# Performance work log

Hardware: AMD Instinct MI355X
Metric: run time of the kernel (lower is better)

## Reference

```python
import jax, jax.numpy as jnp
import numpy as np

B, S, D = 2, 2048, 1024
H = 16
HD = D // H  # 64


def setup_inputs() -> dict:
    key = jax.random.key(0)
    ks = jax.random.split(key, 5)
    scale = 1.0 / np.sqrt(D)
    return {
        "x": jax.random.normal(ks[0], (B, S, D), dtype=jnp.float32),
        "kqv_w": jax.random.normal(ks[1], (3 * D, D), dtype=jnp.float32) * scale,
        "kqv_b": jnp.zeros((3 * D,), dtype=jnp.float32),
        "out_w": jax.random.normal(ks[2], (D, D), dtype=jnp.float32) * scale,
        "out_b": jnp.zeros((D,), dtype=jnp.float32),
    }


def reference(x, kqv_w, kqv_b, out_w, out_b):
    # x: [B, S, D] -> torch code transposes to [S, B, D] (seq-first)
    xs = jnp.transpose(x, (1, 0, 2))  # [S, B, D]
    qkv = xs @ kqv_w.T + kqv_b        # [S, B, 3D]
    q, k, v = jnp.split(qkv, 3, axis=-1)  # each [S, B, D]

    def to_heads(t):
        # [S, B, D] -> [S, B*H, HD] -> [B*H, S, HD]
        return jnp.transpose(t.reshape(S, B * H, HD), (1, 0, 2))

    q, k, v = to_heads(q), to_heads(k), to_heads(v)
    # NOTE: original module computes self.scaling but never applies it -> no q scaling.
    attn = jnp.einsum('nqd,nkd->nqk', q, k)      # [B*H, S, S]
    attn = jax.nn.softmax(attn, axis=-1)
    out = jnp.einsum('nqk,nkd->nqd', attn, v)    # [B*H, S, HD]
    out = jnp.transpose(out, (1, 0, 2)).reshape(S, B, D)  # [S, B, D]
    out = out @ out_w.T + out_b
    return jnp.transpose(out, (1, 0, 2))  # [B, S, D]
```

## Files before the change

kernel.cpp:

```cpp
#include <hip/hip_runtime.h>

#define SEQ   2048
#define DIM   1024
#define NH    16
#define HD    64
#define BH    32
#define TOK   4096

typedef __bf16 bf16;
typedef __attribute__((ext_vector_type(4))) __bf16 bf16x4;
typedef __attribute__((ext_vector_type(8))) __bf16 bf16x8;
typedef __attribute__((ext_vector_type(4))) float f32x4;

#define LOG2E 1.44269504f

__device__ inline f32x4 mfma16(bf16x8 a, bf16x8 b, f32x4 c) {
  return __builtin_amdgcn_mfma_f32_16x16x32_bf16(a, b, c, 0, 0, 0);
}

__device__ inline void gload_lds16(const bf16* g, bf16* lds) {
  __builtin_amdgcn_global_load_lds(
      (const __attribute__((address_space(1))) void*)g,
      (__attribute__((address_space(3))) void*)lds, 16, 0, 0);
}

__device__ inline float exp2_hw(float x) {
  float r;
  asm("v_exp_f32 %0, %1" : "=v"(r) : "v"(x));
  return r;
}

__device__ inline void split8(const float* src, bf16x8& hi, bf16x8& lo) {
  float4 a = *(const float4*)src;
  float4 b = *(const float4*)(src + 4);
  float f[8] = {a.x, a.y, a.z, a.w, b.x, b.y, b.z, b.w};
#pragma unroll
  for (int i = 0; i < 8; ++i) {
    bf16 h = (bf16)f[i];
    hi[i] = h;
    lo[i] = (bf16)(f[i] - (float)h);
  }
}

__device__ inline void cast8(const float* src, bf16* dst) {
  float4 a = *(const float4*)src;
  float4 b = *(const float4*)(src + 4);
  bf16x8 v;
  v[0] = (bf16)a.x; v[1] = (bf16)a.y; v[2] = (bf16)a.z; v[3] = (bf16)a.w;
  v[4] = (bf16)b.x; v[5] = (bf16)b.y; v[6] = (bf16)b.z; v[7] = (bf16)b.w;
  *(bf16x8*)dst = v;
}

__global__ void prep_kernel(const float* __restrict__ x,
                            const float* __restrict__ kqv_w,
                            const float* __restrict__ out_w,
                            bf16* __restrict__ xh, bf16* __restrict__ xl,
                            bf16* __restrict__ wbf, bf16* __restrict__ wout) {
  const int NX8 = TOK * DIM / 8;
  const int NW8 = 3 * DIM * DIM / 8;
  const int NO8 = DIM * DIM / 8;
  int i = blockIdx.x * 256 + threadIdx.x;
  if (i < NX8) {
    bf16x8 h, l;
    split8(x + (size_t)i * 8, h, l);
    ((bf16x8*)xh)[i] = h;
    ((bf16x8*)xl)[i] = l;
  } else if (i < NX8 + NW8) {
    int j = i - NX8;
    cast8(kqv_w + (size_t)j * 8, wbf + (size_t)j * 8);
  } else if (i < NX8 + NW8 + NO8) {
    int j = i - NX8 - NW8;
    cast8(out_w + (size_t)j * 8, wout + (size_t)j * 8);
  }
}

__global__ __launch_bounds__(256) void gemm_qkv_ps(
    const bf16* __restrict__ xh, const bf16* __restrict__ xl,
    const bf16* __restrict__ wbf, const float* __restrict__ bias,
    bf16* __restrict__ qhh, bf16* __restrict__ qhl, bf16* __restrict__ kh,
    bf16* __restrict__ vT) {
  __shared__ bf16 AhA[64 * 64], AlA[64 * 64], BhA[64 * 64];
  __shared__ bf16 AhB[64 * 64], AlB[64 * 64], BhB[64 * 64];
  const int tid = threadIdx.x;
  const int lane = tid & 63;
  const int wave = tid >> 6;
  const int lr = lane & 15, lk = lane >> 4;
  const int bid = blockIdx.x;
  const int swz = (bid & 7) * 96 + (bid >> 3);
  const int m0 = (swz / 24) * 128, n0 = (swz % 24) * 128;
  const bool two_term = (n0 < DIM);
  const int wm = (wave >> 1) * 64, wn = (wave & 1) * 64;
  f32x4 acc[4][4] = {};

  const int c0i = tid, c1i = 256 + tid;
  const int rp0 = c0i >> 3, lc0 = (c0i & 7) ^ (rp0 & 7);
  const int mm0 = (lc0 >> 2) * 64 + rp0, kk0 = (lc0 & 3) * 8;
  const int rp1 = c1i >> 3, lc1 = (c1i & 7) ^ (rp1 & 7);
  const int mm1 = (lc1 >> 2) * 64 + rp1, kk1 = (lc1 & 3) * 8;
  const bf16* pA0 = xh + (size_t)(m0 + mm0) * DIM + kk0;
  const bf16* pA1 = xh + (size_t)(m0 + mm1) * DIM + kk1;
  const bf16* pL0 = xl + (size_t)(m0 + mm0) * DIM + kk0;
  const bf16* pL1 = xl + (size_t)(m0 + mm1) * DIM + kk1;
  const bf16* pB0 = wbf + (size_t)(n0 + mm0) * DIM + kk0;
  const bf16* pB1 = wbf + (size_t)(n0 + mm1) * DIM + kk1;

  auto stageG = [&](bf16* Ah_, bf16* Al_, bf16* Bh_) {
    gload_lds16(pA0, Ah_ + c0i * 8);
    gload_lds16(pA1, Ah_ + c1i * 8);
    if (two_term) {
      gload_lds16(pL0, Al_ + c0i * 8);
      gload_lds16(pL1, Al_ + c1i * 8);
    }
    gload_lds16(pB0, Bh_ + c0i * 8);
    gload_lds16(pB1, Bh_ + c1i * 8);
    pA0 += 32; pA1 += 32; pL0 += 32; pL1 += 32;
    pB0 += 32; pB1 += 32;
  };

  auto computeG = [&](const bf16* Ah, const bf16* Al, const bf16* Bh) {
    bf16x8 afh[4], afl[4], bfv[4];
#pragma unroll
    for (int i = 0; i < 4; ++i) {
      int m = wm + i * 16 + lr;
      int rp = m & 63;
      int pc = ((m >> 6) * 4 + lk) ^ (rp & 7);
      afh[i] = *(const bf16x8*)(Ah + rp * 64 + pc * 8);
    }
#pragma unroll
    for (int j = 0; j < 4; ++j) {
      int m = wn + j * 16 + lr;
      int rp = m & 63;
      int pc = ((m >> 6) * 4 + lk) ^ (rp & 7);
      bfv[j] = *(const bf16x8*)(Bh + rp * 64 + pc * 8);
    }
    __builtin_amdgcn_s_setprio(1);
#pragma unroll
    for (int i = 0; i < 4; ++i)
#pragma unroll
      for (int j = 0; j < 4; ++j)
        acc[i][j] = mfma16(afh[i], bfv[j], acc[i][j]);
    __builtin_amdgcn_s_setprio(0);
    if (two_term) {
#pragma unroll
      for (int i = 0; i < 4; ++i) {
        int m = wm + i * 16 + lr;
        int rp = m & 63;
        int pc = ((m >> 6) * 4 + lk) ^ (rp & 7);
        afl[i] = *(const bf16x8*)(Al + rp * 64 + pc * 8);
      }
      __builtin_amdgcn_s_setprio(1);
#pragma unroll
      for (int i = 0; i < 4; ++i)
#pragma unroll
        for (int j = 0; j < 4; ++j)
          acc[i][j] = mfma16(afl[i], bfv[j], acc[i][j]);
      __builtin_amdgcn_s_setprio(0);
    }
  };

  stageG(AhA, AlA, BhA);
  __syncthreads();
  for (int k0 = 0; k0 < DIM; k0 += 64) {
    stageG(AhB, AlB, BhB);
    computeG(AhA, AlA, BhA);
    __syncthreads();
    if (k0 + 64 < DIM) {
      stageG(AhA, AlA, BhA);
    }
    computeG(AhB, AlB, BhB);
    __syncthreads();
  }

#pragma unroll
  for (int j = 0; j < 4; ++j) {
    int col = n0 + wn + j * 16 + lr;
    float bv = bias[col];
    int part = col >> 10, cc2 = col & 1023;
    int h = cc2 >> 6, d = cc2 & 63;
#pragma unroll
    for (int i = 0; i < 4; ++i) {
      int rowb = m0 + wm + i * 16 + lk * 4;
#pragma unroll
      for (int r = 0; r < 4; ++r) {
        int row = rowb + r;
        float val = acc[i][j][r] + bv;
        int b = row >> 11, s = row & 2047;
        int n = b * NH + h;
        size_t idx = ((size_t)n * SEQ + s) * HD + d;
        if (part == 0) {
          float vq = val * LOG2E;
          bf16 qh_ = (bf16)vq;
          qhh[idx] = qh_;
          qhl[idx] = (bf16)(vq - (float)qh_);
        } else if (part == 1) {
          kh[idx] = (bf16)val;
        } else {
          vT[((size_t)n * HD + d) * SEQ + s] = (bf16)val;
        }
      }
    }
  }
}

__global__ __launch_bounds__(256) void gemm_out(
    const bf16* __restrict__ A, const bf16* __restrict__ Bw,
    const float* __restrict__ bias, float* __restrict__ outF) {
  __shared__ bf16 AsA[64 * 64], BsA[64 * 64];
  __shared__ bf16 AsB[64 * 64], BsB[64 * 64];
  const int tid = threadIdx.x;
  const int lane = tid & 63;
  const int wave = tid >> 6;
  const int lr = lane & 15, lk = lane >> 4;
  const int bid = blockIdx.x;
  const int swz = (bid & 7) * 32 + (bid >> 3);
  const int m0 = (swz >> 3) * 128, n0 = (swz & 7) * 128;
  const int wm = (wave >> 1) * 64, wn = (wave & 1) * 64;
  f32x4 acc[4][4] = {};

  const int c0i = tid, c1i = 256 + tid;
  const int rp0 = c0i >> 3, lc0 = (c0i & 7) ^ (rp0 & 7);
  const int mm0 = (lc0 >> 2) * 64 + rp0, kk0 = (lc0 & 3) * 8;
  const int rp1 = c1i >> 3, lc1 = (c1i & 7) ^ (rp1 & 7);
  const int mm1 = (lc1 >> 2) * 64 + rp1, kk1 = (lc1 & 3) * 8;
  const bf16* pA0 = A + (size_t)(m0 + mm0) * DIM + kk0;
  const bf16* pA1 = A + (size_t)(m0 + mm1) * DIM + kk1;
  const bf16* pB0 = Bw + (size_t)(n0 + mm0) * DIM + kk0;
  const bf16* pB1 = Bw + (size_t)(n0 + mm1) * DIM + kk1;

#define STAGEO(As_, Bs_)              \
  do {                                \
    gload_lds16(pA0, As_ + c0i * 8);  \
    gload_lds16(pA1, As_ + c1i * 8);  \
    gload_lds16(pB0, Bs_ + c0i * 8);  \
    gload_lds16(pB1, Bs_ + c1i * 8);  \
    pA0 += 32; pA1 += 32;             \
    pB0 += 32; pB1 += 32;             \
  } while (0)

  auto computeO = [&](const bf16* As, const bf16* Bs) {
    bf16x8 af[4], bfv[4];
#pragma unroll
    for (int i = 0; i < 4; ++i) {
      int m = wm + i * 16 + lr;
      int rp = m & 63;
      int pc = ((m >> 6) * 4 + lk) ^ (rp & 7);
      af[i] = *(const bf16x8*)(As + rp * 64 + pc * 8);
    }
#pragma unroll
    for (int j = 0; j < 4; ++j) {
      int m = wn + j * 16 + lr;
      int rp = m & 63;
      int pc = ((m >> 6) * 4 + lk) ^ (rp & 7);
      bfv[j] = *(const bf16x8*)(Bs + rp * 64 + pc * 8);
    }
    __builtin_amdgcn_s_setprio(1);
#pragma unroll
    for (int i = 0; i < 4; ++i)
#pragma unroll
      for (int j = 0; j < 4; ++j)
        acc[i][j] = mfma16(af[i], bfv[j], acc[i][j]);
    __builtin_amdgcn_s_setprio(0);
  };

  STAGEO(AsA, BsA);
  __syncthreads();
  for (int k0 = 0; k0 < DIM; k0 += 64) {
    STAGEO(AsB, BsB);
    computeO(AsA, BsA);
    __syncthreads();
    if (k0 + 64 < DIM) {
      STAGEO(AsA, BsA);
    }
    computeO(AsB, BsB);
    __syncthreads();
  }
#undef STAGEO

#pragma unroll
  for (int j = 0; j < 4; ++j) {
    int col = n0 + wn + j * 16 + lr;
    float bv = bias[col];
#pragma unroll
    for (int i = 0; i < 4; ++i) {
      int rowb = m0 + wm + i * 16 + lk * 4;
#pragma unroll
      for (int r = 0; r < 4; ++r)
        outF[(size_t)(rowb + r) * DIM + col] = acc[i][j][r] + bv;
    }
  }
}

__global__ __launch_bounds__(256) void attn_kernel(
    const bf16* __restrict__ qhh, const bf16* __restrict__ qhl,
    const bf16* __restrict__ kh, const bf16* __restrict__ vT,
    bf16* __restrict__ aout) {
  __shared__ bf16 KsA[64 * 64], VsA[64 * 64];
  __shared__ bf16 KsB[64 * 64], VsB[64 * 64];
  const int tid = threadIdx.x;
  const int lane = tid & 63;
  const int w = tid >> 6;
  const int lr = lane & 15, lk = lane >> 4;
  const int bid = blockIdx.x;
  const int swz = (bid & 7) * 64 + (bid >> 3);
  const int n = swz >> 4;
  const int q0 = (swz & 15) * 128 + w * 32;

  const bf16* qbh = qhh + ((size_t)n * SEQ + q0) * HD;
  const bf16* qbl = qhl + ((size_t)n * SEQ + q0) * HD;
  bf16x8 aqh[2][2], aql[2][2];
#pragma unroll
  for (int g = 0; g < 2; ++g) {
    aqh[g][0] = *(const bf16x8*)(qbh + (g * 16 + lr) * HD + lk * 8);
    aqh[g][1] = *(const bf16x8*)(qbh + (g * 16 + lr) * HD + 32 + lk * 8);
    aql[g][0] = *(const bf16x8*)(qbl + (g * 16 + lr) * HD + lk * 8);
    aql[g][1] = *(const bf16x8*)(qbl + (g * 16 + lr) * HD + 32 + lk * 8);
  }

  const int c0i = tid, c1i = 256 + tid;
  const int r0 = c0i >> 3, lc0 = ((c0i & 7) ^ (r0 & 7)) * 8;
  const int r1 = c1i >> 3, lc1 = ((c1i & 7) ^ (r1 & 7)) * 8;
  const size_t kbase = (size_t)n * SEQ * HD;
  const size_t vbase = (size_t)n * HD * SEQ;
  const bf16* pK0 = kh + kbase + (size_t)r0 * HD + lc0;
  const bf16* pK1 = kh + kbase + (size_t)r1 * HD + lc1;
  const bf16* pV0 = vT + vbase + (size_t)r0 * SEQ + lc0;
  const bf16* pV1 = vT + vbase + (size_t)r1 * SEQ + lc1;
  const bool vsw = (w & 1);

  const int u0v = 2 * (lk >> 1) + (lk & 1);
  const int xr = (2 * (lr & 7)) ^ (lr >> 3);
  const int e0 = ((u0v) ^ xr) * 4;
  const int e1 = ((u0v + 4) ^ xr) * 4;
  const int e2 = ((u0v + 8) ^ xr) * 4;
  const int e3 = ((u0v + 12) ^ xr) * 4;

  bf16x8 ones;
#pragma unroll
  for (int i = 0; i < 8; ++i) ones[i] = (bf16)1.0f;

  f32x4 o[2][4] = {};
  float lrow[2][4] = {};

#define STAGE_K(Ks_)                      \
  do {                                    \
    gload_lds16(pK0, Ks_ + c0i * 8);      \
    gload_lds16(pK1, Ks_ + c1i * 8);      \
    pK0 += 64 * HD; pK1 += 64 * HD;       \
  } while (0)

#define VLOAD(a, b)                       \
  do {                                    \
    a = *(const uint4*)pV0;               \
    b = *(const uint4*)pV1;               \
    pV0 += 64; pV1 += 64;                 \
  } while (0)

#define VWRITE(Vs_, a, b)                                      \
  do {                                                         \
    uint4 t0, t1;                                              \
    if (vsw) {                                                 \
      t0.x = a.z; t0.y = a.w; t0.z = a.x; t0.w = a.y;          \
      t1.x = b.z; t1.y = b.w; t1.z = b.x; t1.w = b.y;          \
    } else { t0 = a; t1 = b; }                                 \
    *(uint4*)((char*)(Vs_) + c0i * 16) = t0;                   \
    *(uint4*)((char*)(Vs_) + c1i * 16) = t1;                   \
  } while (0)

  auto compute = [&](const bf16* Ks, const bf16* Vs) {
    f32x4 sa[2][4] = {};
    __builtin_amdgcn_s_setprio(1);
#pragma unroll
    for (int j = 0; j < 4; ++j) {
      int row = j * 16 + lr;
      int c0 = (lk ^ (row & 7)) * 8;
      int c1 = ((4 + lk) ^ (row & 7)) * 8;
      const bf16* kr = Ks + row * 64;
      bf16x8 b0 = *(const bf16x8*)(kr + c0);
      bf16x8 b1 = *(const bf16x8*)(kr + c1);
#pragma unroll
      for (int g = 0; g < 2; ++g) {
        sa[g][j] = mfma16(b0, aqh[g][0], sa[g][j]);
        sa[g][j] = mfma16(b1, aqh[g][1], sa[g][j]);
        sa[g][j] = mfma16(b0, aql[g][0], sa[g][j]);
        sa[g][j] = mfma16(b1, aql[g][1], sa[g][j]);
      }
    }
    __builtin_amdgcn_s_setprio(0);

    bf16x8 pa[2][2];
#pragma unroll
    for (int g = 0; g < 2; ++g)
#pragma unroll
      for (int jj = 0; jj < 2; ++jj)
#pragma unroll
        for (int r = 0; r < 4; ++r) {
          pa[g][0][jj * 4 + r] = (bf16)exp2_hw(sa[g][jj][r]);
          pa[g][1][jj * 4 + r] = (bf16)exp2_hw(sa[g][2 + jj][r]);
        }

    __builtin_amdgcn_s_setprio(1);
    f32x4 ls[2] = {};
#pragma unroll
    for (int g = 0; g < 2; ++g) {
      ls[g] = mfma16(pa[g][0], ones, ls[g]);
      ls[g] = mfma16(pa[g][1], ones, ls[g]);
    }
#pragma unroll
    for (int dj = 0; dj < 4; ++dj) {
      int row = dj * 16 + lr;
      const bf16* vr = Vs + row * 64;
      bf16x4 v00 = *(const bf16x4*)(vr + e0);
      bf16x4 v01 = *(const bf16x4*)(vr + e1);
      bf16x4 v10 = *(const bf16x4*)(vr + e2);
      bf16x4 v11 = *(const bf16x4*)(vr + e3);
      bf16x8 vf0, vf1;
#pragma unroll
      for (int i = 0; i < 4; ++i) {
        vf0[i] = v00[i]; vf0[4 + i] = v01[i];
        vf1[i] = v10[i]; vf1[4 + i] = v11[i];
      }
#pragma unroll
      for (int g = 0; g < 2; ++g) {
        o[g][dj] = mfma16(pa[g][0], vf0, o[g][dj]);
        o[g][dj] = mfma16(pa[g][1], vf1, o[g][dj]);
      }
    }
    __builtin_amdgcn_s_setprio(0);
#pragma unroll
    for (int g = 0; g < 2; ++g)
#pragma unroll
      for (int r = 0; r < 4; ++r) lrow[g][r] += ls[g][r];
  };

  uint4 va0, va1;
  STAGE_K(KsA);
  VLOAD(va0, va1);
  VWRITE(VsA, va0, va1);
  __syncthreads();

  for (int it = 0; it < SEQ / 64; it += 2) {
    STAGE_K(KsB);
    uint4 vb0, vb1;
    VLOAD(vb0, vb1);
    compute(KsA, VsA);
    VWRITE(VsB, vb0, vb1);
    __syncthreads();
    bool more = (it + 2 < SEQ / 64);
    if (more) {
      STAGE_K(KsA);
      VLOAD(va0, va1);
    }
    compute(KsB, VsB);
    if (more) VWRITE(VsA, va0, va1);
    __syncthreads();
  }
#undef STAGE_K
#undef VLOAD
#undef VWRITE

  const int b = n >> 4, h = n & 15;
#pragma unroll
  for (int g = 0; g < 2; ++g)
#pragma unroll
    for (int r = 0; r < 4; ++r) {
      float inv = 1.0f / lrow[g][r];
      int s = q0 + g * 16 + lk * 4 + r;
      size_t base = ((size_t)(b * SEQ + s)) * DIM + h * HD;
#pragma unroll
      for (int j = 0; j < 4; ++j)
        aout[base + j * 16 + lr] = (bf16)(o[g][j][r] * inv);
    }
}

extern "C" void kernel_launch(void* const* d_in, const int* in_sizes, int n_in,
                              void* d_out, int out_size, void* d_ws, size_t ws_size,
                              hipStream_t stream) {
  const float* x     = (const float*)d_in[0];
  const float* kqv_w = (const float*)d_in[1];
  const float* kqv_b = (const float*)d_in[2];
  const float* out_w = (const float*)d_in[3];
  const float* out_b = (const float*)d_in[4];
  float* out = (float*)d_out;

  const size_t NX  = (size_t)TOK * DIM;
  const size_t NW  = (size_t)3 * DIM * DIM;
  const size_t NO  = (size_t)DIM * DIM;
  const size_t NKV = (size_t)BH * SEQ * HD;

  bf16* xh   = (bf16*)d_ws;
  bf16* xl   = xh + NX;
  bf16* wbf  = xl + NX;
  bf16* wout = wbf + NW;
  bf16* qhh  = wout + NO;
  bf16* qhl  = qhh + NKV;
  bf16* kh   = qhl + NKV;
  bf16* vT   = kh + NKV;
  bf16* aout = xh;

  const int PREP_BLOCKS = (int)((NX + NW + NO) / 8 / 256);
  prep_kernel<<<PREP_BLOCKS, 256, 0, stream>>>(x, kqv_w, out_w, xh, xl, wbf, wout);
  gemm_qkv_ps<<<768, 256, 0, stream>>>(xh, xl, wbf, kqv_b, qhh, qhl, kh, vT);
  attn_kernel<<<512, 256, 0, stream>>>(qhh, qhl, kh, vT, aout);
  gemm_out<<<256, 256, 0, stream>>>(aout, wout, out_b, out);
}
```

Before: 135.5 us.

## Pre-permute V tiles in QKV GEMM epilogue for direct async LDS loads

The QKV GEMM epilogue now writes V in a per-64-key-tile layout whose key order is pre-permuted to match the MFMA B-operand fragment order. The attention kernel can then stage V with global_load_lds just like K, instead of register loads, lane-dependent swaps and LDS stores. Each MFMA fragment becomes a single 16-byte LDS read instead of four 8-byte reads plus shuffles. The cost is scattered 2-byte stores of V in the GEMM epilogue, and the LDS reads rely on the XOR swizzle that global_load_lds applies to match the permuted order.

```diff
diff --git a/kernel.cpp b/kernel.cpp
--- a/kernel.cpp
+++ b/kernel.cpp
@@ -78,7 +78,7 @@
     const bf16* __restrict__ xh, const bf16* __restrict__ xl,
     const bf16* __restrict__ wbf, const float* __restrict__ bias,
     bf16* __restrict__ qhh, bf16* __restrict__ qhl, bf16* __restrict__ kh,
-    bf16* __restrict__ vT) {
+    bf16* __restrict__ vP) {
   __shared__ bf16 AhA[64 * 64], AlA[64 * 64], BhA[64 * 64];
   __shared__ bf16 AhB[64 * 64], AlB[64 * 64], BhB[64 * 64];
   const int tid = threadIdx.x;
@@ -195,7 +195,13 @@
         } else if (part == 1) {
           kh[idx] = (bf16)val;
         } else {
-          vT[((size_t)n * HD + d) * SEQ + s] = (bf16)val;
+          int kt = s >> 6;
+          int s6 = s & 63;
+          int p = (s6 >> 5) & 1;
+          int s5 = s6 & 31;
+          int hh = s5 >> 4, l = (s5 >> 2) & 3, rr = s5 & 3;
+          int u = (p * 4 + l) * 8 + hh * 4 + rr;
+          vP[(((size_t)n * 32 + kt) * 64 + d) * 64 + u] = (bf16)val;
         }
       }
     }
@@ -292,7 +298,7 @@
 
 __global__ __launch_bounds__(256) void attn_kernel(
     const bf16* __restrict__ qhh, const bf16* __restrict__ qhl,
-    const bf16* __restrict__ kh, const bf16* __restrict__ vT,
+    const bf16* __restrict__ kh, const bf16* __restrict__ vP,
     bf16* __restrict__ aout) {
   __shared__ bf16 KsA[64 * 64], VsA[64 * 64];
   __shared__ bf16 KsB[64 * 64], VsB[64 * 64];
@@ -320,19 +326,10 @@
   const int r0 = c0i >> 3, lc0 = ((c0i & 7) ^ (r0 & 7)) * 8;
   const int r1 = c1i >> 3, lc1 = ((c1i & 7) ^ (r1 & 7)) * 8;
   const size_t kbase = (size_t)n * SEQ * HD;
-  const size_t vbase = (size_t)n * HD * SEQ;
   const bf16* pK0 = kh + kbase + (size_t)r0 * HD + lc0;
   const bf16* pK1 = kh + kbase + (size_t)r1 * HD + lc1;
-  const bf16* pV0 = vT + vbase + (size_t)r0 * SEQ + lc0;
-  const bf16* pV1 = vT + vbase + (size_t)r1 * SEQ + lc1;
-  const bool vsw = (w & 1);
-
-  const int u0v = 2 * (lk >> 1) + (lk & 1);
-  const int xr = (2 * (lr & 7)) ^ (lr >> 3);
-  const int e0 = ((u0v) ^ xr) * 4;
-  const int e1 = ((u0v + 4) ^ xr) * 4;
-  const int e2 = ((u0v + 8) ^ xr) * 4;
-  const int e3 = ((u0v + 12) ^ xr) * 4;
+  const bf16* pV0 = vP + kbase + (size_t)r0 * 64 + lc0;
+  const bf16* pV1 = vP + kbase + (size_t)r1 * 64 + lc1;
 
   bf16x8 ones;
 #pragma unroll
@@ -341,29 +338,14 @@
   f32x4 o[2][4] = {};
   float lrow[2][4] = {};
 
-#define STAGE_K(Ks_)                      \
+#define STAGE(Ks_, Vs_)                   \
   do {                                    \
     gload_lds16(pK0, Ks_ + c0i * 8);      \
     gload_lds16(pK1, Ks_ + c1i * 8);      \
+    gload_lds16(pV0, Vs_ + c0i * 8);      \
+    gload_lds16(pV1, Vs_ + c1i * 8);      \
     pK0 += 64 * HD; pK1 += 64 * HD;       \
-  } while (0)
-
-#define VLOAD(a, b)                       \
-  do {                                    \
-    a = *(const uint4*)pV0;               \
-    b = *(const uint4*)pV1;               \
-    pV0 += 64; pV1 += 64;                 \
-  } while (0)
-
-#define VWRITE(Vs_, a, b)                                      \
-  do {                                                         \
-    uint4 t0, t1;                                              \
-    if (vsw) {                                                 \
-      t0.x = a.z; t0.y = a.w; t0.z = a.x; t0.w = a.y;          \
-      t1.x = b.z; t1.y = b.w; t1.z = b.x; t1.w = b.y;          \
-    } else { t0 = a; t1 = b; }                                 \
-    *(uint4*)((char*)(Vs_) + c0i * 16) = t0;                   \
-    *(uint4*)((char*)(Vs_) + c1i * 16) = t1;                   \
+    pV0 += 64 * 64; pV1 += 64 * 64;       \
   } while (0)
 
   auto compute = [&](const bf16* Ks, const bf16* Vs) {
@@ -409,20 +391,12 @@
     for (int dj = 0; dj < 4; ++dj) {
       int row = dj * 16 + lr;
       const bf16* vr = Vs + row * 64;
-      bf16x4 v00 = *(const bf16x4*)(vr + e0);
-      bf16x4 v01 = *(const bf16x4*)(vr + e1);
-      bf16x4 v10 = *(const bf16x4*)(vr + e2);
-      bf16x4 v11 = *(const bf16x4*)(vr + e3);
-      bf16x8 vf0, vf1;
-#pragma unroll
-      for (int i = 0; i < 4; ++i) {
-        vf0[i] = v00[i]; vf0[4 + i] = v01[i];
-        vf1[i] = v10[i]; vf1[4 + i] = v11[i];
-      }
-#pragma unroll
-      for (int g = 0; g < 2; ++g) {
-        o[g][dj] = mfma16(pa[g][0], vf0, o[g][dj]);
-        o[g][dj] = mfma16(pa[g][1], vf1, o[g][dj]);
+#pragma unroll
+      for (int p = 0; p < 2; ++p) {
+        bf16x8 vf = *(const bf16x8*)(vr + (((p * 4 + lk) ^ (row & 7)) * 8));
+#pragma unroll
+        for (int g = 0; g < 2; ++g)
+          o[g][dj] = mfma16(pa[g][p], vf, o[g][dj]);
       }
     }
     __builtin_amdgcn_s_setprio(0);
@@ -432,31 +406,20 @@
       for (int r = 0; r < 4; ++r) lrow[g][r] += ls[g][r];
   };
 
-  uint4 va0, va1;
-  STAGE_K(KsA);
-  VLOAD(va0, va1);
-  VWRITE(VsA, va0, va1);
+  STAGE(KsA, VsA);
   __syncthreads();
 
   for (int it = 0; it < SEQ / 64; it += 2) {
-    STAGE_K(KsB);
-    uint4 vb0, vb1;
-    VLOAD(vb0, vb1);
+    STAGE(KsB, VsB);
     compute(KsA, VsA);
-    VWRITE(VsB, vb0, vb1);
-    __syncthreads();
-    bool more = (it + 2 < SEQ / 64);
-    if (more) {
-      STAGE_K(KsA);
-      VLOAD(va0, va1);
+    __syncthreads();
+    if (it + 2 < SEQ / 64) {
+      STAGE(KsA, VsA);
     }
     compute(KsB, VsB);
-    if (more) VWRITE(VsA, va0, va1);
-    __syncthreads();
-  }
-#undef STAGE_K
-#undef VLOAD
-#undef VWRITE
+    __syncthreads();
+  }
+#undef STAGE
 
   const int b = n >> 4, h = n & 15;
 #pragma unroll
@@ -494,12 +457,12 @@
   bf16* qhh  = wout + NO;
   bf16* qhl  = qhh + NKV;
   bf16* kh   = qhl + NKV;
-  bf16* vT   = kh + NKV;
+  bf16* vP   = kh + NKV;
   bf16* aout = xh;
 
   const int PREP_BLOCKS = (int)((NX + NW + NO) / 8 / 256);
   prep_kernel<<<PREP_BLOCKS, 256, 0, stream>>>(x, kqv_w, out_w, xh, xl, wbf, wout);
-  gemm_qkv_ps<<<768, 256, 0, stream>>>(xh, xl, wbf, kqv_b, qhh, qhl, kh, vT);
-  attn_kernel<<<512, 256, 0, stream>>>(qhh, qhl, kh, vT, aout);
+  gemm_qkv_ps<<<768, 256, 0, stream>>>(xh, xl, wbf, kqv_b, qhh, qhl, kh, vP);
+  attn_kernel<<<512, 256, 0, stream>>>(qhh, qhl, kh, vP, aout);
   gemm_out<<<256, 256, 0, stream>>>(aout, wout, out_b, out);
 }
```

New measurement: 132.9 us. No clear change (-1.9%).
